# Kernel optimization log

Measured on AMD Instinct MI355X. Metric: run time of the kernel, lower is better.

The kernel has to match this reference:

```python
import jax, jax.numpy as jnp
import numpy as np

B, P, KN, D, H = 4, 1024, 16, 768, 12
HD = D // H
S = P + 1


def setup_inputs() -> dict:
    key = jax.random.key(0)
    ks = jax.random.split(key, 8)
    s = 0.02
    return {
        "x": jax.random.normal(ks[0], (B, S, D), jnp.float32),
        "routes": jax.random.randint(ks[1], (P, KN), 0, P),
        "qkv_w": jax.random.normal(ks[2], (D, 3 * D), jnp.float32) * s,
        "qkv_b": jnp.zeros((3 * D,), jnp.float32),
        "proj_w": jax.random.normal(ks[3], (D, D), jnp.float32) * s,
        "proj_b": jnp.zeros((D,), jnp.float32),
        "ln1_g": jnp.ones((D,), jnp.float32),
        "ln1_b": jnp.zeros((D,), jnp.float32),
        "ln2_g": jnp.ones((D,), jnp.float32),
        "ln2_b": jnp.zeros((D,), jnp.float32),
        "mlp_w1": jax.random.normal(ks[4], (D, 4 * D), jnp.float32) * s,
        "mlp_b1": jnp.zeros((4 * D,), jnp.float32),
        "mlp_w2": jax.random.normal(ks[5], (4 * D, D), jnp.float32) * s,
        "mlp_b2": jnp.zeros((D,), jnp.float32),
    }


def _ln(x, g, b):
    m = jnp.mean(x, axis=-1, keepdims=True)
    v = jnp.var(x, axis=-1, keepdims=True)
    return (x - m) / jnp.sqrt(v + 1e-5) * g + b


def reference(x, routes, qkv_w, qkv_b, proj_w, proj_b, ln1_g, ln1_b, ln2_g, ln2_b, mlp_w1, mlp_b1, mlp_w2, mlp_b2):
    Bx, Sx, Dx = x.shape
    scale = HD ** -0.5
    xn = _ln(x, ln1_g, ln1_b)
    qkv = (xn @ qkv_w + qkv_b).reshape(Bx, Sx, 3, H, HD).transpose(2, 0, 3, 1, 4)
    Q, K, V = qkv[0], qkv[1], qkv[2]  # each [B,H,S,hd]
    # CLS token: dense attention over all S tokens
    sc_cls = jnp.einsum('bhqd,bhkd->bhqk', Q[:, :, :1], K) * scale
    out_cls = jnp.einsum('bhqk,bhkd->bhqd', jax.nn.softmax(sc_cls, axis=-1), V)
    # Patch tokens: sparse kNN attention via route gather (shift +1 to skip CLS)
    r = routes + 1  # [P,k] indices into S axis
    Kg = K[:, :, r, :]  # [B,H,P,k,hd]
    Vg = V[:, :, r, :]
    sc_p = jnp.einsum('bhpd,bhpkd->bhpk', Q[:, :, 1:], Kg) * scale
    out_p = jnp.einsum('bhpk,bhpkd->bhpd', jax.nn.softmax(sc_p, axis=-1), Vg)
    out = jnp.concatenate([out_cls, out_p], axis=2).transpose(0, 2, 1, 3).reshape(Bx, Sx, Dx)
    x = x + (out @ proj_w + proj_b)
    h = _ln(x, ln2_g, ln2_b)
    h = jax.nn.gelu(h @ mlp_w1 + mlp_b1, approximate=False) @ mlp_w2 + mlp_b2
    return x + h
```

## Files before the change

### kernel.cpp

```cpp
#include <hip/hip_runtime.h>
#include <hip/hip_bf16.h>
#include <cmath>

#define B_ 4
#define P_ 1024
#define KN_ 16
#define D_ 768
#define H_ 12
#define S_ 1025
#define NROWS (B_ * S_)
#define NC_ 32
#define CH_ 33

typedef __attribute__((ext_vector_type(8))) short short8;
typedef __attribute__((ext_vector_type(4))) float f32x4;

__device__ __forceinline__ float bf2f(short u) {
  return __uint_as_float(((unsigned int)(unsigned short)u) << 16);
}

__device__ __forceinline__ float wave_reduce_sum(float v) {
#pragma unroll
  for (int off = 32; off > 0; off >>= 1) v += __shfl_xor(v, off);
  return v;
}

__device__ __forceinline__ void gload16(const void* g, void* l) {
  __builtin_amdgcn_global_load_lds(
      (const __attribute__((address_space(1))) unsigned int*)g,
      (__attribute__((address_space(3))) unsigned int*)l, 16, 0, 0);
}

__global__ __launch_bounds__(256) void ln_bf16(const float* __restrict__ x,
                                               const float* __restrict__ g,
                                               const float* __restrict__ b,
                                               __hip_bfloat16* __restrict__ y) {
  const int row = blockIdx.x;
  const float* xr = x + (size_t)row * D_;
  __hip_bfloat16* yr = y + (size_t)row * D_;
  const int t = threadIdx.x;
  const float v0 = xr[t], v1 = xr[t + 256], v2 = xr[t + 512];
  float s = v0 + v1 + v2;
  float ss = v0 * v0 + v1 * v1 + v2 * v2;
  s = wave_reduce_sum(s);
  ss = wave_reduce_sum(ss);
  __shared__ float rs[4], rss[4];
  const int wid = t >> 6, lane = t & 63;
  if (lane == 0) { rs[wid] = s; rss[wid] = ss; }
  __syncthreads();
  const float tot = rs[0] + rs[1] + rs[2] + rs[3];
  const float tot2 = rss[0] + rss[1] + rss[2] + rss[3];
  const float mean = tot * (1.0f / D_);
  const float var = tot2 * (1.0f / D_) - mean * mean;
  const float rstd = rsqrtf(var + 1e-5f);
  yr[t]       = __float2bfloat16((v0 - mean) * rstd * g[t]       + b[t]);
  yr[t + 256] = __float2bfloat16((v1 - mean) * rstd * g[t + 256] + b[t + 256]);
  yr[t + 512] = __float2bfloat16((v2 - mean) * rstd * g[t + 512] + b[t + 512]);
}

__global__ __launch_bounds__(256) void wtrans(const float* __restrict__ W,
                                              __hip_bfloat16* __restrict__ WT,
                                              int K, int N) {
  __shared__ float t[32][33];
  const int tx = threadIdx.x & 31, ty = threadIdx.x >> 5;
  const int n0 = blockIdx.x * 32, k0 = blockIdx.y * 32;
#pragma unroll
  for (int i = 0; i < 32; i += 8)
    t[ty + i][tx] = W[(size_t)(k0 + ty + i) * N + n0 + tx];
  __syncthreads();
#pragma unroll
  for (int i = 0; i < 32; i += 8)
    WT[(size_t)(n0 + ty + i) * K + k0 + tx] = __float2bfloat16(t[tx][ty + i]);
}

#define STAGE(AS, BS, kt)                                                      \
  {                                                                            \
    _Pragma("unroll")                                                          \
    for (int q = 0; q < 4; ++q)                                                \
      gload16(A + (size_t)(m0 + w * 32 + q * 8 + lrow8) * K + (kt) * 64 +      \
                  lchk * 8,                                                    \
              &AS[w * 32 + q * 8][0]);                                         \
    _Pragma("unroll")                                                          \
    for (int q = 0; q < 2; ++q)                                                \
      gload16(WT + (size_t)(n0 + w * 16 + q * 8 + lrow8) * K + (kt) * 64 +     \
                  lchk * 8,                                                    \
              &BS[w * 16 + q * 8][0]);                                         \
  }

#define COMPUTE(AS, BS)                                                        \
  {                                                                            \
    short8 af[4][2], bfr[2][2];                                                \
    _Pragma("unroll")                                                          \
    for (int i = 0; i < 4; ++i) {                                              \
      _Pragma("unroll")                                                        \
      for (int s = 0; s < 2; ++s) {                                            \
        const int ra = wr * 64 + i * 16 + fr;                                  \
        af[i][s] = *(const short8*)&AS[ra][((s * 4 + fk) ^ (ra & 7)) * 8];     \
      }                                                                        \
    }                                                                          \
    _Pragma("unroll")                                                          \
    for (int j = 0; j < 2; ++j) {                                              \
      _Pragma("unroll")                                                        \
      for (int s = 0; s < 2; ++s) {                                            \
        const int rb = wc * 32 + j * 16 + fr;                                  \
        bfr[j][s] = *(const short8*)&BS[rb][((s * 4 + fk) ^ (rb & 7)) * 8];    \
      }                                                                        \
    }                                                                          \
    _Pragma("unroll")                                                          \
    for (int i = 0; i < 4; ++i) {                                              \
      _Pragma("unroll")                                                        \
      for (int j = 0; j < 2; ++j) {                                            \
        _Pragma("unroll")                                                      \
        for (int s = 0; s < 2; ++s)                                            \
          acc[i][j] = __builtin_amdgcn_mfma_f32_16x16x32_bf16(                 \
              af[i][s], bfr[j][s], acc[i][j], 0, 0, 0);                        \
      }                                                                        \
    }                                                                          \
  }

template <int EPI>
__global__ __launch_bounds__(256) void gemm_mfma(
    const __hip_bfloat16* __restrict__ A, const __hip_bfloat16* __restrict__ WT,
    const float* __restrict__ bias, const float* __restrict__ resid,
    void* __restrict__ Cv, int M, int N, int K) {
  __shared__ __align__(16) __hip_bfloat16 As0[128][64], As1[128][64];
  __shared__ __align__(16) __hip_bfloat16 Bs0[64][64], Bs1[64][64];
  const int tid = threadIdx.x;
  const int l = tid & 63, w = tid >> 6;
  const int wr = w >> 1, wc = w & 1;
  const int fr = l & 15, fk = l >> 4;
  const int lrow8 = l >> 3;
  const int lchk = (l & 7) ^ lrow8;
  const int m0 = blockIdx.y * 128, n0 = blockIdx.x * 64;

  f32x4 acc[4][2] = {};
  const int nk = K >> 6;

  STAGE(As0, Bs0, 0);
  __syncthreads();
  int kt = 0;
  for (; kt + 2 < nk; kt += 2) {
    STAGE(As1, Bs1, kt + 1);
    COMPUTE(As0, Bs0);
    __syncthreads();
    STAGE(As0, Bs0, kt + 2);
    COMPUTE(As1, Bs1);
    __syncthreads();
  }
  STAGE(As1, Bs1, kt + 1);
  COMPUTE(As0, Bs0);
  __syncthreads();
  COMPUTE(As1, Bs1);

#pragma unroll
  for (int i = 0; i < 4; ++i) {
#pragma unroll
    for (int j = 0; j < 2; ++j) {
#pragma unroll
      for (int rg = 0; rg < 4; ++rg) {
        const int m = m0 + wr * 64 + i * 16 + fk * 4 + rg;
        const int n = n0 + wc * 32 + j * 16 + fr;
        if (m < M) {
          float v = acc[i][j][rg] + bias[n];
          if (EPI == 1) v += resid[(size_t)m * N + n];
          if (EPI == 2) v = 0.5f * v * (1.f + erff(v * 0.70710678118654752f));
          if (EPI == 1) ((float*)Cv)[(size_t)m * N + n] = v;
          else ((__hip_bfloat16*)Cv)[(size_t)m * N + n] = __float2bfloat16(v);
        }
      }
    }
  }
}

__global__ __launch_bounds__(256) void attn_cls_part(
    const __hip_bfloat16* __restrict__ qkv, float* __restrict__ part) {
  const int bh = blockIdx.x / NC_, chunk = blockIdx.x % NC_;
  const int b = bh / H_, h = bh % H_;
  const int c0 = chunk * CH_;
  const int nk = min(CH_, S_ - c0);
  __shared__ float qs[64];
  __shared__ float sc[CH_];
  __shared__ float redm, redl;
  __shared__ float pl[4][64];
  const int t = threadIdx.x;
  const int wid = t >> 6, lane = t & 63;
  const int rowbase = b * S_;
  if (t < 64) qs[t] = __bfloat162float(qkv[(size_t)rowbase * 2304 + h * 64 + t]);
  __syncthreads();

  if (t < nk) {
    const short8* kp8 =
        (const short8*)(qkv + (size_t)(rowbase + c0 + t) * 2304 + 768 + h * 64);
    float d = 0.f;
#pragma unroll
    for (int i = 0; i < 8; ++i) {
      const short8 v = kp8[i];
#pragma unroll
      for (int j = 0; j < 8; ++j) d += qs[i * 8 + j] * bf2f(v[j]);
    }
    sc[t] = d * 0.125f;
  }
  __syncthreads();
  if (wid == 0) {
    float v = (lane < nk) ? sc[lane] : -1e30f;
    float m = v;
#pragma unroll
    for (int off = 32; off > 0; off >>= 1) m = fmaxf(m, __shfl_xor(m, off));
    float e = (lane < nk) ? expf(v - m) : 0.f;
    if (lane < nk) sc[lane] = e;
    const float lsum = wave_reduce_sum(e);
    if (lane == 0) { redm = m; redl = lsum; }
  }
  __syncthreads();

  float acc = 0.f;
  for (int k = wid; k < nk; k += 4)
    acc += sc[k] *
           __bfloat162float(qkv[(size_t)(rowbase + c0 + k) * 2304 + 1536 + h * 64 + lane]);
  pl[wid][lane] = acc;
  __syncthreads();
  float* po = part + (size_t)(bh * NC_ + chunk) * 68;
  if (t < 64) po[2 + t] = pl[0][t] + pl[1][t] + pl[2][t] + pl[3][t];
  else if (t == 64) po[0] = redm;
  else if (t == 65) po[1] = redl;
}

__global__ __launch_bounds__(64) void attn_cls_merge(
    const float* __restrict__ part, __hip_bfloat16* __restrict__ out) {
  const int bh = blockIdx.x;
  const int b = bh / H_, h = bh % H_;
  const int lane = threadIdx.x;
  const float* pb = part + (size_t)bh * NC_ * 68;
  float M = -1e30f;
#pragma unroll
  for (int i = 0; i < NC_; ++i) M = fmaxf(M, pb[i * 68]);
  float den = 0.f, o = 0.f;
#pragma unroll
  for (int i = 0; i < NC_; ++i) {
    const float wgt = expf(pb[i * 68] - M);
    den += wgt * pb[i * 68 + 1];
    o += wgt * pb[i * 68 + 2 + lane];
  }
  out[(size_t)(b * S_) * 768 + h * 64 + lane] = __float2bfloat16(o / den);
}

__global__ __launch_bounds__(256) void attn_patch(const __hip_bfloat16* __restrict__ qkv,
                                                  const int* __restrict__ routes,
                                                  __hip_bfloat16* __restrict__ out) {
  const int gwid = (int)((blockIdx.x * 256 + threadIdx.x) >> 6);
  const int lane = threadIdx.x & 63;
  const int p = gwid & (P_ - 1);
  const int bh = gwid >> 10;
  const int h = bh % H_, b = bh / H_;
  const int qrow = b * S_ + p + 1;
  const int j = lane >> 2, s = lane & 3;

  const short8* qp = (const short8*)(qkv + (size_t)qrow * 2304 + h * 64 + s * 16);
  const short8 q0 = qp[0], q1 = qp[1];
  float qf[16];
#pragma unroll
  for (int i = 0; i < 8; ++i) { qf[i] = bf2f(q0[i]); qf[8 + i] = bf2f(q1[i]); }

  const int krow = b * S_ + routes[p * KN_ + j] + 1;

  const short8* kp = (const short8*)(qkv + (size_t)krow * 2304 + 768 + h * 64 + s * 16);
  const short8 k0 = kp[0], k1 = kp[1];
  float d = 0.f;
#pragma unroll
  for (int i = 0; i < 8; ++i) { d += qf[i] * bf2f(k0[i]); d += qf[8 + i] * bf2f(k1[i]); }
  d += __shfl_xor(d, 1);
  d += __shfl_xor(d, 2);
  d *= 0.125f;

  float mx = d;
#pragma unroll
  for (int off = 4; off <= 32; off <<= 1) mx = fmaxf(mx, __shfl_xor(mx, off));
  const float e = expf(d - mx);
  float den = e;
#pragma unroll
  for (int off = 4; off <= 32; off <<= 1) den += __shfl_xor(den, off);
  const float inv = 1.f / den;

  float o = 0.f;
#pragma unroll
  for (int jj = 0; jj < KN_; ++jj) {
    const float ej = __shfl(e, jj * 4);
    const int krj = __shfl(krow, jj * 4);
    o += ej * __bfloat162float(qkv[(size_t)krj * 2304 + 1536 + h * 64 + lane]);
  }
  out[(size_t)qrow * 768 + h * 64 + lane] = __float2bfloat16(o * inv);
}

extern "C" void kernel_launch(void* const* d_in, const int* in_sizes, int n_in,
                              void* d_out, int out_size, void* d_ws, size_t ws_size,
                              hipStream_t stream) {
  const float* x      = (const float*)d_in[0];
  const int*   routes = (const int*)d_in[1];
  const float* qkv_w  = (const float*)d_in[2];
  const float* qkv_b  = (const float*)d_in[3];
  const float* proj_w = (const float*)d_in[4];
  const float* proj_b = (const float*)d_in[5];
  const float* ln1_g  = (const float*)d_in[6];
  const float* ln1_b  = (const float*)d_in[7];
  const float* ln2_g  = (const float*)d_in[8];
  const float* ln2_b  = (const float*)d_in[9];
  const float* mlp_w1 = (const float*)d_in[10];
  const float* mlp_b1 = (const float*)d_in[11];
  const float* mlp_w2 = (const float*)d_in[12];
  const float* mlp_b2 = (const float*)d_in[13];
  float* outp = (float*)d_out;

  __hip_bfloat16* xn    = (__hip_bfloat16*)d_ws;
  __hip_bfloat16* qkv   = xn + (size_t)NROWS * 768;
  __hip_bfloat16* attn  = qkv + (size_t)NROWS * 2304;
  float*          x1    = (float*)(attn + (size_t)NROWS * 768);
  __hip_bfloat16* h1    = (__hip_bfloat16*)(x1 + (size_t)NROWS * 768);
  __hip_bfloat16* wqkvT = h1 + (size_t)NROWS * 3072;
  __hip_bfloat16* wprojT= wqkvT + (size_t)2304 * 768;
  __hip_bfloat16* w1T   = wprojT + (size_t)768 * 768;
  __hip_bfloat16* w2T   = w1T + (size_t)3072 * 768;
  float*          clsp  = (float*)(w2T + (size_t)768 * 3072);

  const int mt = (NROWS + 127) / 128;

  wtrans<<<dim3(2304 / 32, 768 / 32), 256, 0, stream>>>(qkv_w, wqkvT, 768, 2304);
  wtrans<<<dim3(768 / 32, 768 / 32), 256, 0, stream>>>(proj_w, wprojT, 768, 768);
  wtrans<<<dim3(3072 / 32, 768 / 32), 256, 0, stream>>>(mlp_w1, w1T, 768, 3072);
  wtrans<<<dim3(768 / 32, 3072 / 32), 256, 0, stream>>>(mlp_w2, w2T, 3072, 768);

  ln_bf16<<<NROWS, 256, 0, stream>>>(x, ln1_g, ln1_b, xn);
  gemm_mfma<0><<<dim3(2304 / 64, mt), 256, 0, stream>>>(
      xn, wqkvT, qkv_b, nullptr, qkv, NROWS, 2304, 768);
  attn_cls_part<<<B_ * H_ * NC_, 256, 0, stream>>>(qkv, clsp);
  attn_cls_merge<<<B_ * H_, 64, 0, stream>>>(clsp, attn);
  attn_patch<<<B_ * H_ * P_ / 4, 256, 0, stream>>>(qkv, routes, attn);
  gemm_mfma<1><<<dim3(768 / 64, mt), 256, 0, stream>>>(
      attn, wprojT, proj_b, x, x1, NROWS, 768, 768);
  ln_bf16<<<NROWS, 256, 0, stream>>>(x1, ln2_g, ln2_b, xn);
  gemm_mfma<2><<<dim3(3072 / 64, mt), 256, 0, stream>>>(
      xn, w1T, mlp_b1, nullptr, h1, NROWS, 3072, 768);
  gemm_mfma<1><<<dim3(768 / 64, mt), 256, 0, stream>>>(
      h1, w2T, mlp_b2, x1, outp, NROWS, 768, 3072);
}
```

Baseline: 301.9 us.

## Add 128x128 square-tile GEMM for wide GEMMs and XCD-aware block swizzle

Adds a gemm_sq kernel with 128x128 output tiles and a K-step of 32, each wave computing a 64x64 sub-tile, and uses it for the QKV and MLP-up GEMMs. This raises arithmetic intensity per LDS load, since it reuses more B operands. All GEMMs switch to a 1D grid remapped by an XCD-aware swizzle so neighbouring tiles land on the same XCD and share L2. The larger tile means fewer workgroups and more accumulator registers, which may reduce occupancy.

New measurement: 330.7 us. +9.5%, slower.

```diff
diff --git a/kernel.cpp b/kernel.cpp
--- a/kernel.cpp
+++ b/kernel.cpp
@@ -29,6 +29,12 @@
   __builtin_amdgcn_global_load_lds(
       (const __attribute__((address_space(1))) unsigned int*)g,
       (__attribute__((address_space(3))) unsigned int*)l, 16, 0, 0);
+}
+
+__device__ __forceinline__ int xcd_swz(int bid, int nwg) {
+  const int q8 = nwg >> 3, r8 = nwg & 7;
+  const int xcd = bid & 7, pos = bid >> 3;
+  return (xcd < r8 ? xcd * (q8 + 1) : r8 * (q8 + 1) + (xcd - r8) * q8) + pos;
 }
 
 __global__ __launch_bounds__(256) void ln_bf16(const float* __restrict__ x,
@@ -122,7 +128,7 @@
 __global__ __launch_bounds__(256) void gemm_mfma(
     const __hip_bfloat16* __restrict__ A, const __hip_bfloat16* __restrict__ WT,
     const float* __restrict__ bias, const float* __restrict__ resid,
-    void* __restrict__ Cv, int M, int N, int K) {
+    void* __restrict__ Cv, int M, int N, int K, int nx) {
   __shared__ __align__(16) __hip_bfloat16 As0[128][64], As1[128][64];
   __shared__ __align__(16) __hip_bfloat16 Bs0[64][64], Bs1[64][64];
   const int tid = threadIdx.x;
@@ -131,7 +137,8 @@
   const int fr = l & 15, fk = l >> 4;
   const int lrow8 = l >> 3;
   const int lchk = (l & 7) ^ lrow8;
-  const int m0 = blockIdx.y * 128, n0 = blockIdx.x * 64;
+  const int wgid = xcd_swz(blockIdx.x, gridDim.x);
+  const int m0 = (wgid / nx) * 128, n0 = (wgid % nx) * 64;
 
   f32x4 acc[4][2] = {};
   const int nk = K >> 6;
@@ -160,6 +167,91 @@
       for (int rg = 0; rg < 4; ++rg) {
         const int m = m0 + wr * 64 + i * 16 + fk * 4 + rg;
         const int n = n0 + wc * 32 + j * 16 + fr;
+        if (m < M) {
+          float v = acc[i][j][rg] + bias[n];
+          if (EPI == 1) v += resid[(size_t)m * N + n];
+          if (EPI == 2) v = 0.5f * v * (1.f + erff(v * 0.70710678118654752f));
+          if (EPI == 1) ((float*)Cv)[(size_t)m * N + n] = v;
+          else ((__hip_bfloat16*)Cv)[(size_t)m * N + n] = __float2bfloat16(v);
+        }
+      }
+    }
+  }
+}
+
+#define SQSTAGE(AS, BS, kt)                                                    \
+  {                                                                            \
+    _Pragma("unroll")                                                          \
+    for (int q = 0; q < 2; ++q) {                                              \
+      const int s = w * 2 + q;                                                 \
+      const int r = s * 16 + srow;                                             \
+      const int c = schunk ^ ((r >> 1) & 3);                                   \
+      gload16(A + (size_t)(m0 + r) * K + (kt) * 32 + c * 8, &AS[s * 16][0]);   \
+      gload16(WT + (size_t)(n0 + r) * K + (kt) * 32 + c * 8, &BS[s * 16][0]);  \
+    }                                                                          \
+  }
+
+#define SQCOMPUTE(AS, BS)                                                      \
+  {                                                                            \
+    short8 af[4], bfr[4];                                                      \
+    _Pragma("unroll")                                                          \
+    for (int i = 0; i < 4; ++i) {                                              \
+      const int ra = wr * 64 + i * 16 + lrow;                                  \
+      af[i] = *(const short8*)&AS[ra][(lk ^ ((ra >> 1) & 3)) * 8];             \
+      const int rb = wc * 64 + i * 16 + lrow;                                  \
+      bfr[i] = *(const short8*)&BS[rb][(lk ^ ((rb >> 1) & 3)) * 8];            \
+    }                                                                          \
+    _Pragma("unroll")                                                          \
+    for (int i = 0; i < 4; ++i) {                                              \
+      _Pragma("unroll")                                                        \
+      for (int j = 0; j < 4; ++j)                                              \
+        acc[i][j] = __builtin_amdgcn_mfma_f32_16x16x32_bf16(                   \
+            af[i], bfr[j], acc[i][j], 0, 0, 0);                                \
+    }                                                                          \
+  }
+
+template <int EPI>
+__global__ __launch_bounds__(256) void gemm_sq(
+    const __hip_bfloat16* __restrict__ A, const __hip_bfloat16* __restrict__ WT,
+    const float* __restrict__ bias, const float* __restrict__ resid,
+    void* __restrict__ Cv, int M, int N, int K, int nx) {
+  __shared__ __align__(16) __hip_bfloat16 As0[128][32], As1[128][32];
+  __shared__ __align__(16) __hip_bfloat16 Bs0[128][32], Bs1[128][32];
+  const int tid = threadIdx.x;
+  const int l = tid & 63, w = tid >> 6;
+  const int wr = w >> 1, wc = w & 1;
+  const int lrow = l & 15, lk = l >> 4;
+  const int srow = l >> 2, schunk = l & 3;
+  const int wgid = xcd_swz(blockIdx.x, gridDim.x);
+  const int m0 = (wgid / nx) * 128, n0 = (wgid % nx) * 128;
+
+  f32x4 acc[4][4] = {};
+  const int nk = K >> 5;
+
+  SQSTAGE(As0, Bs0, 0);
+  __syncthreads();
+  int kt = 0;
+  for (; kt + 2 < nk; kt += 2) {
+    SQSTAGE(As1, Bs1, kt + 1);
+    SQCOMPUTE(As0, Bs0);
+    __syncthreads();
+    SQSTAGE(As0, Bs0, kt + 2);
+    SQCOMPUTE(As1, Bs1);
+    __syncthreads();
+  }
+  SQSTAGE(As1, Bs1, kt + 1);
+  SQCOMPUTE(As0, Bs0);
+  __syncthreads();
+  SQCOMPUTE(As1, Bs1);
+
+#pragma unroll
+  for (int i = 0; i < 4; ++i) {
+#pragma unroll
+    for (int j = 0; j < 4; ++j) {
+#pragma unroll
+      for (int rg = 0; rg < 4; ++rg) {
+        const int m = m0 + wr * 64 + i * 16 + lk * 4 + rg;
+        const int n = n0 + wc * 64 + j * 16 + lrow;
         if (m < M) {
           float v = acc[i][j][rg] + bias[n];
           if (EPI == 1) v += resid[(size_t)m * N + n];
@@ -329,16 +421,16 @@
   wtrans<<<dim3(768 / 32, 3072 / 32), 256, 0, stream>>>(mlp_w2, w2T, 3072, 768);
 
   ln_bf16<<<NROWS, 256, 0, stream>>>(x, ln1_g, ln1_b, xn);
-  gemm_mfma<0><<<dim3(2304 / 64, mt), 256, 0, stream>>>(
-      xn, wqkvT, qkv_b, nullptr, qkv, NROWS, 2304, 768);
+  gemm_sq<0><<<(2304 / 128) * mt, 256, 0, stream>>>(
+      xn, wqkvT, qkv_b, nullptr, qkv, NROWS, 2304, 768, 2304 / 128);
   attn_cls_part<<<B_ * H_ * NC_, 256, 0, stream>>>(qkv, clsp);
   attn_cls_merge<<<B_ * H_, 64, 0, stream>>>(clsp, attn);
   attn_patch<<<B_ * H_ * P_ / 4, 256, 0, stream>>>(qkv, routes, attn);
-  gemm_mfma<1><<<dim3(768 / 64, mt), 256, 0, stream>>>(
-      attn, wprojT, proj_b, x, x1, NROWS, 768, 768);
+  gemm_mfma<1><<<(768 / 64) * mt, 256, 0, stream>>>(
+      attn, wprojT, proj_b, x, x1, NROWS, 768, 768, 768 / 64);
   ln_bf16<<<NROWS, 256, 0, stream>>>(x1, ln2_g, ln2_b, xn);
-  gemm_mfma<2><<<dim3(3072 / 64, mt), 256, 0, stream>>>(
-      xn, w1T, mlp_b1, nullptr, h1, NROWS, 3072, 768);
-  gemm_mfma<1><<<dim3(768 / 64, mt), 256, 0, stream>>>(
-      h1, w2T, mlp_b2, x1, outp, NROWS, 768, 3072);
-}
+  gemm_sq<2><<<(3072 / 128) * mt, 256, 0, stream>>>(
+      xn, w1T, mlp_b1, nullptr, h1, NROWS, 3072, 768, 3072 / 128);
+  gemm_mfma<1><<<(768 / 64) * mt, 256, 0, stream>>>(
+      h1, w2T, mlp_b2, x1, outp, NROWS, 768, 3072, 768 / 64);
+}
```
